# Kernel tuning notes

Hardware: AMD Instinct MI355X
Metric: run time of the kernel (lower is better)

The kernel has to match this reference:

```python
import jax, jax.numpy as jnp
import numpy as np

VOCAB = 50257
EMB = 1024
HID = 1024
B, T = 8, 256


def setup_inputs() -> dict:
    key = jax.random.key(0)
    ks = jax.random.split(key, 6)
    s = 0.05  # small init scale for numerical sanity
    return {
        "x": jax.random.randint(ks[0], (B, T), 0, VOCAB, dtype=jnp.int64) if jax.config.jax_enable_x64 else jax.random.randint(ks[0], (B, T), 0, VOCAB, dtype=jnp.int32),
        "emb_W": jax.random.normal(ks[1], (VOCAB, EMB), dtype=jnp.float32) * s,
        "W_ih": jax.random.normal(ks[2], (4 * HID, EMB), dtype=jnp.float32) * s,
        "W_hh": jax.random.normal(ks[3], (4 * HID, HID), dtype=jnp.float32) * s,
        "b_ih": jax.random.normal(ks[4], (4 * HID,), dtype=jnp.float32) * s,
        "b_hh": jax.random.normal(ks[5], (4 * HID,), dtype=jnp.float32) * s,
        "dec_b": jnp.zeros((VOCAB,), dtype=jnp.float32),
    }


def _lstm(emb, W_ih, W_hh, b_ih, b_hh):
    # emb: [B, T, E]. Precompute input projections for all timesteps (one big GEMM).
    x_proj = jnp.einsum("bte,ge->btg", emb, W_ih) + (b_ih + b_hh)  # [B, T, 4H]
    h0 = jnp.zeros((emb.shape[0], HID), emb.dtype)
    c0 = jnp.zeros((emb.shape[0], HID), emb.dtype)

    def step(carry, xt):  # xt: [B, 4H]
        h, c = carry
        g = xt + h @ W_hh.T  # [B, 4H]
        i, f, gg, o = jnp.split(g, 4, axis=-1)  # PyTorch gate order i,f,g,o
        i = jax.nn.sigmoid(i)
        f = jax.nn.sigmoid(f)
        gg = jnp.tanh(gg)
        o = jax.nn.sigmoid(o)
        c_new = f * c + i * gg
        h_new = o * jnp.tanh(c_new)
        return (h_new, c_new), h_new

    (hT, cT), hs = jax.lax.scan(step, (h0, c0), jnp.swapaxes(x_proj, 0, 1))
    out = jnp.swapaxes(hs, 0, 1)  # [B, T, H], batch_first
    return out, (hT[None], cT[None])  # num_layers=1 leading dim


def reference(x, emb_W, W_ih, W_hh, b_ih, b_hh, dec_b):
    emb = emb_W[x]                                   # [B, T, E]
    out, hidden = _lstm(emb, W_ih, W_hh, b_ih, b_hh)  # [B, T, H]
    logits = jnp.einsum("bth,vh->btv", out, emb_W) + dec_b  # tied decoder
    logits = logits.reshape(-1, VOCAB)
    return jax.nn.log_softmax(logits, axis=1), hidden
```

## Files before the change

### kernel.cpp

```cpp
#include <hip/hip_runtime.h>

typedef float f32x4 __attribute__((ext_vector_type(4)));
typedef __bf16 bf16x8 __attribute__((ext_vector_type(8)));
typedef unsigned int u32x4 __attribute__((ext_vector_type(4)));
typedef unsigned short u16;
typedef unsigned int u32;

#define VOCAB 50257
#define KDIM 1024
#define MROWS 2048
#define TSEQ 256
#define NBLK 64
#define NTILE 393
#define NT (NTILE * 2)
#define LOGN ((size_t)MROWS * VOCAB)

__device__ __forceinline__ u16 f2bf(float f) {
    u32 u = __builtin_bit_cast(u32, f);
    u = (u + 0x7FFFu + ((u >> 16) & 1u)) >> 16;
    return (u16)u;
}

__device__ __forceinline__ float sigm(float x) { return 1.0f / (1.0f + __expf(-x)); }

__device__ __forceinline__ u32 min4u(u32x4 v) {
    u32 a = v.x < v.y ? v.x : v.y;
    u32 b = v.z < v.w ? v.z : v.w;
    return a < b ? a : b;
}

__device__ __forceinline__ ushort4 cvt4(float4 v) {
    ushort4 o;
    o.x = f2bf(v.x); o.y = f2bf(v.y); o.z = f2bf(v.z); o.w = f2bf(v.w);
    return o;
}


#define PB_GATH 8192
#define PB_HSEQ 10240
#define PB_BIAS 14352
#define PB_EMBW 14368
#define PB_EMBW_N 8192
#define PREP_BLOCKS (PB_EMBW + PB_EMBW_N)

__global__ __launch_bounds__(256)
void prep_all(const float4* __restrict__ Wih, ushort4* __restrict__ Wih_bf,
              const float4* __restrict__ Whh, ushort4* __restrict__ Whh_bf,
              const int* __restrict__ x, const float* __restrict__ embW,
              ushort4* __restrict__ emb_bf, u32* __restrict__ hseq,
              const float* __restrict__ bih, const float* __restrict__ bhh,
              float* __restrict__ bsum, ushort4* __restrict__ embW_bf)
{
    const int bid = blockIdx.x, tid = threadIdx.x;
    if (bid < 4096) {
        long i = (long)bid * 256 + tid;
        Wih_bf[i] = cvt4(Wih[i]);
    } else if (bid < PB_GATH) {
        long i = (long)(bid - 4096) * 256 + tid;
        Whh_bf[i] = cvt4(Whh[i]);
    } else if (bid < PB_HSEQ) {
        int m = bid - PB_GATH;
        int row = x[m];
        float4 v = ((const float4*)(embW + (size_t)row * KDIM))[tid];
        emb_bf[(size_t)m * 256 + tid] = cvt4(v);
    } else if (bid < PB_BIAS) {
        int i = (bid - PB_HSEQ) * 256 + tid;
        hseq[i] = (i < 4096) ? 0x00010001u : 0u;
    } else if (bid < PB_EMBW) {
        int i = (bid - PB_BIAS) * 256 + tid;
        if (i < 4096) bsum[i] = bih[i] + bhh[i];
    } else {
        long i = (long)(bid - PB_EMBW) * 256 + tid;
        const long n4 = (long)VOCAB * KDIM / 4;
        const long stride = (long)PB_EMBW_N * 256;
        const float4* src = (const float4*)embW;
        for (; i < n4; i += stride) embW_bf[i] = cvt4(src[i]);
    }
}


#define BM 128
#define BN 128
#define BK 64

__device__ __forceinline__ void gl_lds16(const u16* g, const u16* l) {
    __builtin_amdgcn_global_load_lds(
        (const __attribute__((address_space(1))) u32*)g,
        (__attribute__((address_space(3))) u32*)l, 16, 0, 0);
}

__global__ __launch_bounds__(256, 2)
void gemm_bt(const u16* __restrict__ A, const u16* __restrict__ Bm,
             const float* __restrict__ bias, float* __restrict__ C,
             int N, int Nb, int K, int ldc)
{
    __shared__ __align__(16) u16 As[BM * BK];
    __shared__ __align__(16) u16 Bs[BN * BK];
    const int tid  = threadIdx.x;
    const int lane = tid & 63;
    const int wid  = tid >> 6;

    const int gx  = gridDim.x;
    const int nwg = gx * gridDim.y;
    const int lin = blockIdx.y * gx + blockIdx.x;
    const int qq = nwg >> 3, rr = nwg & 7;
    const int xcd = lin & 7, idx = lin >> 3;
    const int neu = (xcd < rr) ? (xcd * (qq + 1) + idx)
                               : (rr * (qq + 1) + (xcd - rr) * qq + idx);
    const int bm = neu % gx;
    const int bn = neu / gx;

    const int wr = wid >> 1, wc = wid & 1;

    const u16* gA[4]; const u16* gB[4];
    const u16* ldsA[4]; const u16* ldsB[4];
#pragma unroll
    for (int r = 0; r < 4; ++r) {
        int L = r * 256 + tid;
        int row = L >> 3, ps = L & 7;
        int ls = ps ^ (row & 7);
        gA[r] = A + (size_t)(bm * BM + row) * K + ls * 8;
        int brow = bn * BN + row; brow = brow < Nb ? brow : Nb - 1;
        gB[r] = Bm + (size_t)brow * K + ls * 8;
        ldsA[r] = As + (r * 256 + wid * 64) * 8;
        ldsB[r] = Bs + (r * 256 + wid * 64) * 8;
    }

    const int lrow = lane & 15, ksl = lane >> 4;
    int aoff[4][2], boff[4][2];
#pragma unroll
    for (int i = 0; i < 4; ++i)
#pragma unroll
        for (int ks = 0; ks < 2; ++ks) {
            int ar = wr * 64 + i * 16 + lrow;
            aoff[i][ks] = ar * BK + (((ks * 4 + ksl) ^ (ar & 7)) * 8);
            int br = wc * 64 + i * 16 + lrow;
            boff[i][ks] = br * BK + (((ks * 4 + ksl) ^ (br & 7)) * 8);
        }

    f32x4 acc[4][4] = {};
    for (int kt = 0; kt < K; kt += BK) {
#pragma unroll
        for (int r = 0; r < 4; ++r) gl_lds16(gA[r] + kt, ldsA[r]);
#pragma unroll
        for (int r = 0; r < 4; ++r) gl_lds16(gB[r] + kt, ldsB[r]);
        __syncthreads();
        bf16x8 af[4][2], bfb[4][2];
#pragma unroll
        for (int i = 0; i < 4; ++i)
#pragma unroll
            for (int ks = 0; ks < 2; ++ks) {
                af[i][ks]  = *(const bf16x8*)(As + aoff[i][ks]);
                bfb[i][ks] = *(const bf16x8*)(Bs + boff[i][ks]);
            }
#pragma unroll
        for (int ks = 0; ks < 2; ++ks)
#pragma unroll
            for (int mi = 0; mi < 4; ++mi)
#pragma unroll
                for (int ni = 0; ni < 4; ++ni)
                    acc[mi][ni] = __builtin_amdgcn_mfma_f32_16x16x32_bf16(
                        af[mi][ks], bfb[ni][ks], acc[mi][ni], 0, 0, 0);
        __syncthreads();
    }

    const int crl = lane >> 4, ccl = lane & 15;
    const int row0 = bm * BM + wr * 64, col0 = bn * BN + wc * 64;
#pragma unroll
    for (int ni = 0; ni < 4; ++ni) {
        int col = col0 + ni * 16 + ccl;
        if (col < N) {
            float bv = bias[col];
#pragma unroll
            for (int mi = 0; mi < 4; ++mi) {
                int row = row0 + mi * 16 + crl * 4;
                float* cp = C + (size_t)row * ldc + col;
#pragma unroll
                for (int r = 0; r < 4; ++r)
                    cp[(size_t)r * ldc] = acc[mi][ni][r] + bv;
            }
        }
    }
}


__global__ __launch_bounds__(256, 3)
void gemm_dec(const u16* __restrict__ A, const u16* __restrict__ Bm,
              const float* __restrict__ bias, u16* __restrict__ Cb,
              float* __restrict__ pmax, float* __restrict__ psum)
{
    const int N = VOCAB, Nb = VOCAB, K = KDIM;
    __shared__ __align__(16) u16 As[BM * BK];
    __shared__ __align__(16) u16 Bs[BN * BK];
    const int tid  = threadIdx.x;
    const int lane = tid & 63;
    const int wid  = tid >> 6;

    const int gx  = gridDim.x;
    const int nwg = gx * gridDim.y;
    const int lin = blockIdx.y * gx + blockIdx.x;
    const int qq = nwg >> 3, rr = nwg & 7;
    const int xcd = lin & 7, idx = lin >> 3;
    const int neu = (xcd < rr) ? (xcd * (qq + 1) + idx)
                               : (rr * (qq + 1) + (xcd - rr) * qq + idx);
    const int bm = neu % gx;
    const int bn = neu / gx;

    const int wr = wid >> 1, wc = wid & 1;

    const u16* gA[4]; const u16* gB[4];
    const u16* ldsA[4]; const u16* ldsB[4];
#pragma unroll
    for (int r = 0; r < 4; ++r) {
        int L = r * 256 + tid;
        int row = L >> 3, ps = L & 7;
        int ls = ps ^ (row & 7);
        gA[r] = A + (size_t)(bm * BM + row) * K + ls * 8;
        int brow = bn * BN + row; brow = brow < Nb ? brow : Nb - 1;
        gB[r] = Bm + (size_t)brow * K + ls * 8;
        ldsA[r] = As + (r * 256 + wid * 64) * 8;
        ldsB[r] = Bs + (r * 256 + wid * 64) * 8;
    }

    const int lrow = lane & 15, ksl = lane >> 4;
    int aoff[4][2], boff[4][2];
#pragma unroll
    for (int i = 0; i < 4; ++i)
#pragma unroll
        for (int ks = 0; ks < 2; ++ks) {
            int ar = wr * 64 + i * 16 + lrow;
            aoff[i][ks] = ar * BK + (((ks * 4 + ksl) ^ (ar & 7)) * 8);
            int br = wc * 64 + i * 16 + lrow;
            boff[i][ks] = br * BK + (((ks * 4 + ksl) ^ (br & 7)) * 8);
        }

    f32x4 acc[4][4] = {};
    for (int kt = 0; kt < K; kt += BK) {
#pragma unroll
        for (int r = 0; r < 4; ++r) gl_lds16(gA[r] + kt, ldsA[r]);
#pragma unroll
        for (int r = 0; r < 4; ++r) gl_lds16(gB[r] + kt, ldsB[r]);
        __syncthreads();
        bf16x8 af[4][2], bfb[4][2];
#pragma unroll
        for (int i = 0; i < 4; ++i)
#pragma unroll
            for (int ks = 0; ks < 2; ++ks) {
                af[i][ks]  = *(const bf16x8*)(As + aoff[i][ks]);
                bfb[i][ks] = *(const bf16x8*)(Bs + boff[i][ks]);
            }
#pragma unroll
        for (int ks = 0; ks < 2; ++ks)
#pragma unroll
            for (int mi = 0; mi < 4; ++mi)
#pragma unroll
                for (int ni = 0; ni < 4; ++ni)
                    acc[mi][ni] = __builtin_amdgcn_mfma_f32_16x16x32_bf16(
                        af[mi][ks], bfb[ni][ks], acc[mi][ni], 0, 0, 0);
        __syncthreads();
    }

    const int crl = lane >> 4, ccl = lane & 15;
    const int row0 = bm * BM + wr * 64, col0 = bn * BN + wc * 64;
    float bve[4]; bool vld[4];
#pragma unroll
    for (int ni = 0; ni < 4; ++ni) {
        int col = col0 + ni * 16 + ccl;
        vld[ni] = col < N;
        bve[ni] = vld[ni] ? bias[col] : 0.f;
    }
#pragma unroll
    for (int ni = 0; ni < 4; ++ni) {
        if (vld[ni]) {
            int col = col0 + ni * 16 + ccl;
#pragma unroll
            for (int mi = 0; mi < 4; ++mi) {
                int row = row0 + mi * 16 + crl * 4;
                u16* cp = Cb + (size_t)row * (VOCAB * 2) + col;
#pragma unroll
                for (int r = 0; r < 4; ++r)
                    cp[(size_t)r * (VOCAB * 2)] = f2bf(acc[mi][ni][r] + bve[ni]);
            }
        }
    }
#pragma unroll
    for (int mi = 0; mi < 4; ++mi)
#pragma unroll
        for (int r = 0; r < 4; ++r) {
            int row = row0 + mi * 16 + crl * 4 + r;
            float v0 = vld[0] ? acc[mi][0][r] + bve[0] : -3.0e38f;
            float v1 = vld[1] ? acc[mi][1][r] + bve[1] : -3.0e38f;
            float v2 = vld[2] ? acc[mi][2][r] + bve[2] : -3.0e38f;
            float v3 = vld[3] ? acc[mi][3][r] + bve[3] : -3.0e38f;
            float rmax = fmaxf(fmaxf(v0, v1), fmaxf(v2, v3));
#pragma unroll
            for (int m2 = 1; m2 < 16; m2 <<= 1) rmax = fmaxf(rmax, __shfl_xor(rmax, m2));
            float rs = __expf(v0 - rmax) + __expf(v1 - rmax) +
                       __expf(v2 - rmax) + __expf(v3 - rmax);
#pragma unroll
            for (int m2 = 1; m2 < 16; m2 <<= 1) rs += __shfl_xor(rs, m2);
            if (ccl == 0) {
                pmax[(size_t)row * NT + bn * 2 + wc] = rmax;
                psum[(size_t)row * NT + bn * 2 + wc] = rs;
            }
        }
}


__global__ __launch_bounds__(256, 1)
void lstm_persist(const u16* __restrict__ Whh,
                  const float* __restrict__ xproj,
                  u16* __restrict__ hseq,
                  u16* __restrict__ hall,
                  float* __restrict__ outTail)
{
    const int tid = threadIdx.x;
    const int bid = blockIdx.x;

    const int lane = tid & 63;
    const int wq   = tid >> 6;
    const int lrow = lane & 15, ksl = lane >> 4;
    const int colbase = bid * 16;

    bf16x8 Bf[32];
    {
        const u16* bp = Whh + (size_t)(wq * 1024 + colbase + lrow) * KDIM + ksl * 8;
#pragma unroll
        for (int kk = 0; kk < 32; ++kk)
            asm volatile("global_load_dwordx4 %0, %1, off"
                         : "=v"(Bf[kk]) : "v"(bp + kk * 32));
        asm volatile("s_waitcnt vmcnt(0)" ::: "memory");
        __builtin_amdgcn_sched_barrier(0);
    }

    __shared__ float S[4][8][16];
    __shared__ __align__(16) u16 hstage[2][16384];

    for (int i = tid; i < 2 * 64 * 8; i += 256) {
        int buf = i >> 9, rem = i & 511;
        int j = rem >> 3, rowoff = rem & 7;
        u32x4 z = {0, 0, 0, 0};
        *(u32x4*)(&hstage[buf][j * 256 + 128 + rowoff * 16]) = z;
        *(u32x4*)(&hstage[buf][j * 256 + 128 + rowoff * 16 + 8]) = z;
    }

    const bool upd = tid < 128;
    const int b8 = tid >> 4, c16 = tid & 15;
    float creg = 0.f;
    float xp0 = 0.f, xp1 = 0.f, xp2 = 0.f, xp3 = 0.f;
    size_t xbase = 0;
    if (upd) {
        xbase = (size_t)b8 * TSEQ * 4096 + colbase + c16;
        xp0 = xproj[xbase];          xp1 = xproj[xbase + 1024];
        xp2 = xproj[xbase + 2048];   xp3 = xproj[xbase + 3072];
    }

    const int pj = tid >> 2, pr = (tid & 3) * 2;
    const int sw = (pj & 7) << 3;
    int widx[4];
#pragma unroll
    for (int k = 0; k < 4; ++k)
        widx[k] = pj * 256 + ((pr * 16 + k * 8) ^ sw);

    int aro[4];
#pragma unroll
    for (int i = 0; i < 4; ++i) {
        int swr = ((2 * i + (ksl >> 1)) & 7) << 3;
        aro[i] = (ksl >> 1) * 256 + ((lrow * 16 + (ksl & 1) * 8) ^ swr);
    }

    for (int t = 0; t < TSEQ; ++t) {
        const u32* src = (const u32*)hseq + (size_t)t * 4096 + pj * 64 + pr * 8;
        u32x4 P0, P1, P2, P3;
        for (;;) {
            asm volatile("global_load_dwordx4 %0, %1, off sc0 sc1" : "=v"(P0) : "v"(src));
            asm volatile("global_load_dwordx4 %0, %1, off sc0 sc1" : "=v"(P1) : "v"(src + 4));
            asm volatile("global_load_dwordx4 %0, %1, off sc0 sc1" : "=v"(P2) : "v"(src + 8));
            asm volatile("global_load_dwordx4 %0, %1, off sc0 sc1" : "=v"(P3) : "v"(src + 12));
            asm volatile("s_waitcnt vmcnt(0)" ::: "memory");
            __builtin_amdgcn_sched_barrier(0);
            u32 a = min4u(P0), b = min4u(P1), c = min4u(P2), d = min4u(P3);
            u32 mn = (a < b ? a : b); u32 mn2 = (c < d ? c : d);
            if ((mn < mn2 ? mn : mn2) != 0u) break;
        }
        {
            u16* hb2 = &hstage[t & 1][0];
            *(u32x4*)(hb2 + widx[0]) = P0;
            *(u32x4*)(hb2 + widx[1]) = P1;
            *(u32x4*)(hb2 + widx[2]) = P2;
            *(u32x4*)(hb2 + widx[3]) = P3;
        }
        __syncthreads();

        const u16* sb = &hstage[t & 1][0];
        f32x4 ac0 = {}, ac1 = {}, ac2 = {}, ac3 = {};
#pragma unroll
        for (int g = 0; g < 8; ++g) {
            bf16x8 a0 = *(const bf16x8*)(sb + g * 2048 + 0 * 512 + aro[0]);
            bf16x8 a1 = *(const bf16x8*)(sb + g * 2048 + 1 * 512 + aro[1]);
            bf16x8 a2 = *(const bf16x8*)(sb + g * 2048 + 2 * 512 + aro[2]);
            bf16x8 a3 = *(const bf16x8*)(sb + g * 2048 + 3 * 512 + aro[3]);
            ac0 = __builtin_amdgcn_mfma_f32_16x16x32_bf16(a0, Bf[g * 4 + 0], ac0, 0, 0, 0);
            ac1 = __builtin_amdgcn_mfma_f32_16x16x32_bf16(a1, Bf[g * 4 + 1], ac1, 0, 0, 0);
            ac2 = __builtin_amdgcn_mfma_f32_16x16x32_bf16(a2, Bf[g * 4 + 2], ac2, 0, 0, 0);
            ac3 = __builtin_amdgcn_mfma_f32_16x16x32_bf16(a3, Bf[g * 4 + 3], ac3, 0, 0, 0);
        }
        if (ksl < 2) {
#pragma unroll
            for (int r = 0; r < 4; ++r)
                S[wq][ksl * 4 + r][lrow] = ac0[r] + ac1[r] + ac2[r] + ac3[r];
        }
        __syncthreads();

        if (upd) {
            float gi = S[0][b8][c16] + xp0;
            float gf = S[1][b8][c16] + xp1;
            float gg = S[2][b8][c16] + xp2;
            float go = S[3][b8][c16] + xp3;
            float iv = sigm(gi), fv = sigm(gf), ov = sigm(go);
            float gv = tanhf(gg);
            creg = fv * creg + iv * gv;
            float hv = ov * tanhf(creg);
            u16 hbx = f2bf(hv) | 1;
            int w0 = (int)hbx;
            int w1 = __shfl_down(w0, 1);
            if (!(c16 & 1)) {
                u32 wp = (u32)(u16)w0 | ((u32)(u16)w1 << 16);
                u32* dst = (u32*)hseq + (size_t)(t + 1) * 4096 + bid * 64 + b8 * 8 + (c16 >> 1);
                __hip_atomic_store(dst, wp, __ATOMIC_RELAXED, __HIP_MEMORY_SCOPE_AGENT);
                u32* hd = (u32*)hall
                          + ((((size_t)b8 * TSEQ + t) * KDIM + colbase + c16) >> 1);
                *hd = wp;
            }
            if (t == TSEQ - 1) {
                outTail[b8 * KDIM + colbase + c16] = hv;
                outTail[8192 + b8 * KDIM + colbase + c16] = creg;
            }
            int tn = (t + 1 < TSEQ) ? t + 1 : t;
            size_t xb = xbase + (size_t)tn * 4096;
            xp0 = xproj[xb];        xp1 = xproj[xb + 1024];
            xp2 = xproj[xb + 2048]; xp3 = xproj[xb + 3072];
        }
    }
}


__global__ __launch_bounds__(256)
void merge_final(const float* __restrict__ pmax, const float* __restrict__ psum,
                 float* __restrict__ out)
{
    const int m = blockIdx.x;
    const int tid = threadIdx.x;
    __shared__ float smx[4], ssm[4], slse;

    float mx = -3.0e38f, s = 0.f;
    for (int i = tid; i < NT; i += 256) {
        float pm = pmax[(size_t)m * NT + i];
        float ps = psum[(size_t)m * NT + i];
        if (pm > mx) { s *= __expf(mx - pm); mx = pm; }
        s += ps * __expf(pm - mx);
    }
#pragma unroll
    for (int off = 32; off > 0; off >>= 1) {
        float om = __shfl_xor(mx, off), os = __shfl_xor(s, off);
        float nm = fmaxf(mx, om);
        s = s * __expf(mx - nm) + os * __expf(om - nm);
        mx = nm;
    }
    if ((tid & 63) == 0) { smx[tid >> 6] = mx; ssm[tid >> 6] = s; }
    __syncthreads();
    if (tid == 0) {
        float M = fmaxf(fmaxf(smx[0], smx[1]), fmaxf(smx[2], smx[3]));
        float S4 = ssm[0] * __expf(smx[0] - M) + ssm[1] * __expf(smx[1] - M) +
                   ssm[2] * __expf(smx[2] - M) + ssm[3] * __expf(smx[3] - M);
        slse = M + __logf(S4);
    }
    __syncthreads();
    const float L = slse;

    const u32* srcw = (const u32*)out + (size_t)m * VOCAB;
    float* dst = out + (size_t)m * VOCAB;
    const int NCH = (VOCAB + 2047) / 2048;
    for (int c = NCH - 1; c >= 0; --c) {
        int e0 = c * 2048 + tid * 8;
        int w0i = e0 >> 1;
        u32 w0 = srcw[w0i], w1 = srcw[w0i + 1], w2 = srcw[w0i + 2], w3 = srcw[w0i + 3];
        __syncthreads();
        float f[8];
        f[0] = __builtin_bit_cast(float, (w0 & 0xFFFFu) << 16) - L;
        f[1] = __builtin_bit_cast(float, w0 & 0xFFFF0000u) - L;
        f[2] = __builtin_bit_cast(float, (w1 & 0xFFFFu) << 16) - L;
        f[3] = __builtin_bit_cast(float, w1 & 0xFFFF0000u) - L;
        f[4] = __builtin_bit_cast(float, (w2 & 0xFFFFu) << 16) - L;
        f[5] = __builtin_bit_cast(float, w2 & 0xFFFF0000u) - L;
        f[6] = __builtin_bit_cast(float, (w3 & 0xFFFFu) << 16) - L;
        f[7] = __builtin_bit_cast(float, w3 & 0xFFFF0000u) - L;
        if (e0 + 8 <= VOCAB) {
#pragma unroll
            for (int k = 0; k < 8; ++k) dst[e0 + k] = f[k];
        } else {
#pragma unroll
            for (int k = 0; k < 8; ++k) if (e0 + k < VOCAB) dst[e0 + k] = f[k];
        }
    }
}


extern "C" void kernel_launch(void* const* d_in, const int* in_sizes, int n_in,
                              void* d_out, int out_size, void* d_ws, size_t ws_size,
                              hipStream_t stream)
{
    const int*   x    = (const int*)d_in[0];
    const float* embW = (const float*)d_in[1];
    const float* Wih  = (const float*)d_in[2];
    const float* Whh  = (const float*)d_in[3];
    const float* bih  = (const float*)d_in[4];
    const float* bhh  = (const float*)d_in[5];
    const float* decb = (const float*)d_in[6];
    float* out = (float*)d_out;

    char* p = (char*)d_ws;
    auto carve = [&](size_t bytes) {
        char* q = p;
        p += (bytes + 255) & ~(size_t)255;
        return q;
    };
    u16*   embW_bf = (u16*)carve((size_t)VOCAB * KDIM * 2);
    u16*   Wih_bf  = (u16*)carve((size_t)4096 * KDIM * 2);
    u16*   Whh_bf  = (u16*)carve((size_t)4096 * KDIM * 2);
    u16*   emb_bf  = (u16*)carve((size_t)MROWS * KDIM * 2);
    float* xproj   = (float*)carve((size_t)MROWS * 4096 * 4);
    u16*   hall_bf = (u16*)carve((size_t)MROWS * KDIM * 2);
    u16*   hseq    = (u16*)carve((size_t)(TSEQ + 1) * 4096 * 4);
    float* pmax    = (float*)carve((size_t)MROWS * NT * 4);
    float* psum    = (float*)carve((size_t)MROWS * NT * 4);
    float* bsum    = (float*)carve((size_t)4096 * 4);

    prep_all<<<PREP_BLOCKS, 256, 0, stream>>>((const float4*)Wih, (ushort4*)Wih_bf,
                                              (const float4*)Whh, (ushort4*)Whh_bf,
                                              x, embW, (ushort4*)emb_bf,
                                              (u32*)hseq, bih, bhh, bsum,
                                              (ushort4*)embW_bf);

    {
        dim3 g(MROWS / BM, 4096 / BN);
        gemm_bt<<<g, 256, 0, stream>>>(emb_bf, Wih_bf, bsum, xproj, 4096, 4096, KDIM, 4096);
    }

    lstm_persist<<<NBLK, 256, 0, stream>>>(Whh_bf, xproj, hseq, hall_bf, out + LOGN);

    {
        dim3 g(MROWS / BM, NTILE);
        gemm_dec<<<g, 256, 0, stream>>>(hall_bf, embW_bf, decb, (u16*)out, pmax, psum);
    }

    merge_final<<<MROWS, 256, 0, stream>>>(pmax, psum, out);
}
```

Measured before the change: 1.230 ms.

## Overlap embedding weight bf16 conversion with input projection GEMM

Moves the large fp32-to-bf16 conversion of the tied embedding/decoder weight out of the prep kernel and into extra blocks of the input-projection GEMM launch. The GEMM grid gains 16 extra block rows that only perform the conversion and exit, so the bandwidth-bound conversion runs alongside the compute-bound GEMM instead of serially before it. The XCD swizzle now uses a fixed GEMM block count. The risk is that conversion blocks compete with the GEMM for bandwidth and CU slots, and that converting with fewer threads lengthens the tail.

Result: slower. 1.313 ms (+6.7%).

```diff
diff --git a/kernel.cpp b/kernel.cpp
--- a/kernel.cpp
+++ b/kernel.cpp
@@ -39,9 +39,7 @@
 #define PB_GATH 8192
 #define PB_HSEQ 10240
 #define PB_BIAS 14352
-#define PB_EMBW 14368
-#define PB_EMBW_N 8192
-#define PREP_BLOCKS (PB_EMBW + PB_EMBW_N)
+#define PREP_BLOCKS 14368
 
 __global__ __launch_bounds__(256)
 void prep_all(const float4* __restrict__ Wih, ushort4* __restrict__ Wih_bf,
@@ -49,7 +47,7 @@
               const int* __restrict__ x, const float* __restrict__ embW,
               ushort4* __restrict__ emb_bf, u32* __restrict__ hseq,
               const float* __restrict__ bih, const float* __restrict__ bhh,
-              float* __restrict__ bsum, ushort4* __restrict__ embW_bf)
+              float* __restrict__ bsum)
 {
     const int bid = blockIdx.x, tid = threadIdx.x;
     if (bid < 4096) {
@@ -66,15 +64,9 @@
     } else if (bid < PB_BIAS) {
         int i = (bid - PB_HSEQ) * 256 + tid;
         hseq[i] = (i < 4096) ? 0x00010001u : 0u;
-    } else if (bid < PB_EMBW) {
+    } else {
         int i = (bid - PB_BIAS) * 256 + tid;
         if (i < 4096) bsum[i] = bih[i] + bhh[i];
-    } else {
-        long i = (long)(bid - PB_EMBW) * 256 + tid;
-        const long n4 = (long)VOCAB * KDIM / 4;
-        const long stride = (long)PB_EMBW_N * 256;
-        const float4* src = (const float4*)embW;
-        for (; i < n4; i += stride) embW_bf[i] = cvt4(src[i]);
     }
 }
 
@@ -82,6 +74,8 @@
 #define BM 128
 #define BN 128
 #define BK 64
+#define GBY 32
+#define HBY 16
 
 __device__ __forceinline__ void gl_lds16(const u16* g, const u16* l) {
     __builtin_amdgcn_global_load_lds(
@@ -90,18 +84,29 @@
 }
 
 __global__ __launch_bounds__(256, 2)
-void gemm_bt(const u16* __restrict__ A, const u16* __restrict__ Bm,
-             const float* __restrict__ bias, float* __restrict__ C,
-             int N, int Nb, int K, int ldc)
+void gemm_bt_conv(const u16* __restrict__ A, const u16* __restrict__ Bm,
+                  const float* __restrict__ bias, float* __restrict__ C,
+                  int N, int Nb, int K, int ldc,
+                  const float4* __restrict__ embW, ushort4* __restrict__ embW_bf)
 {
+    const int tid  = threadIdx.x;
+
+    if (blockIdx.y >= GBY) {
+        long hb = (long)(blockIdx.y - GBY) * gridDim.x + blockIdx.x;
+        long i = hb * 256 + tid;
+        const long n4 = (long)VOCAB * KDIM / 4;
+        const long stride = (long)HBY * gridDim.x * 256;
+        for (; i < n4; i += stride) embW_bf[i] = cvt4(embW[i]);
+        return;
+    }
+
     __shared__ __align__(16) u16 As[BM * BK];
     __shared__ __align__(16) u16 Bs[BN * BK];
-    const int tid  = threadIdx.x;
     const int lane = tid & 63;
     const int wid  = tid >> 6;
 
     const int gx  = gridDim.x;
-    const int nwg = gx * gridDim.y;
+    const int nwg = gx * GBY;
     const int lin = blockIdx.y * gx + blockIdx.x;
     const int qq = nwg >> 3, rr = nwg & 7;
     const int xcd = lin & 7, idx = lin >> 3;
@@ -539,12 +544,13 @@
     prep_all<<<PREP_BLOCKS, 256, 0, stream>>>((const float4*)Wih, (ushort4*)Wih_bf,
                                               (const float4*)Whh, (ushort4*)Whh_bf,
                                               x, embW, (ushort4*)emb_bf,
-                                              (u32*)hseq, bih, bhh, bsum,
-                                              (ushort4*)embW_bf);
+                                              (u32*)hseq, bih, bhh, bsum);
 
     {
-        dim3 g(MROWS / BM, 4096 / BN);
-        gemm_bt<<<g, 256, 0, stream>>>(emb_bf, Wih_bf, bsum, xproj, 4096, 4096, KDIM, 4096);
+        dim3 g(MROWS / BM, GBY + HBY);
+        gemm_bt_conv<<<g, 256, 0, stream>>>(emb_bf, Wih_bf, bsum, xproj,
+                                            4096, 4096, KDIM, 4096,
+                                            (const float4*)embW, (ushort4*)embW_bf);
     }
 
     lstm_persist<<<NBLK, 256, 0, stream>>>(Whh_bf, xproj, hseq, hall_bf, out + LOGN);
```
